# Optimization experiments

Hardware: AMD Instinct MI355X
Metric: run time of the kernel (lower is better)

## Reference

```python
import jax, jax.numpy as jnp
import numpy as np

H, C, PQ, PV, CZ, CS = 12, 16, 4, 8, 128, 384
W_C = (2.0 / (9.0 * PQ)) ** 0.5
INV_SQRT3 = 3.0 ** -0.5


def setup_inputs() -> dict:
    key = jax.random.key(0)
    ks = jax.random.split(key, 20)
    B, N = 2, 512
    s = jax.random.normal(ks[0], (B, N, CS), jnp.float32)
    z = jax.random.normal(ks[1], (B, N, N, CZ), jnp.float32)
    m = jax.random.normal(ks[2], (B, N, 3, 3), jnp.float32)
    rot, _ = jnp.linalg.qr(m)  # proper-ish rotations (orthonormal frames)
    trans = jax.random.normal(ks[3], (B, N, 3), jnp.float32)
    seq_mask = jnp.ones((B, N), jnp.float32)
    sc = 0.02
    params = {
        'Wq': jax.random.normal(ks[4], (CS, H * C)) * sc,
        'bq': jnp.zeros((H * C,)),
        'Wkv': jax.random.normal(ks[5], (CS, H * C * 2)) * sc,
        'bkv': jnp.zeros((H * C * 2,)),
        'Wb': jax.random.normal(ks[6], (CZ, H)) * sc,
        'bb': jnp.zeros((H,)),
        'Wqp': jax.random.normal(ks[7], (CS, 3 * PQ * H)) * sc,
        'bqp': jnp.zeros((3 * PQ * H,)),
        'Wkvp': jax.random.normal(ks[8], (CS, 3 * (PQ + PV) * H)) * sc,
        'bkvp': jnp.zeros((3 * (PQ + PV) * H,)),
        'gamma': jnp.zeros((H,)),
        'Wout': jax.random.normal(ks[9], ((CZ + C + PV * 4) * H, CS)) * sc,
        'bout': jnp.zeros((CS,)),
    }
    return dict(s=s, z=z, rot=rot, trans=trans, seq_mask=seq_mask, **params)


def reference(s, z, rot, trans, seq_mask, Wq, bq, Wkv, bkv, Wb, bb, Wqp, bqp, Wkvp, bkvp, gamma, Wout, bout):
    B, N, _ = s.shape
    # scalar q/k/v
    q = (s @ Wq + bq).reshape(B, N, H, C)
    kv = (s @ Wkv + bkv).reshape(B, N, H, 2 * C)
    k, v = kv[..., :C], kv[..., C:]
    qp = s @ Wqp + bqp                                   # (B,N,3*PQ*H)
    qp = jnp.stack(jnp.split(qp, 3, axis=-1), axis=-1)   # (B,N,PQ*H,3)
    qp = jnp.einsum('bixy,bipy->bipx', rot, qp) + trans[:, :, None, :]
    qp = qp.reshape(B, N, H, PQ, 3)
    # key/value points
    kvp = s @ Wkvp + bkvp
    kvp = jnp.stack(jnp.split(kvp, 3, axis=-1), axis=-1)  # (B,N,(PQ+PV)*H,3)
    kvp = jnp.einsum('bixy,bipy->bipx', rot, kvp) + trans[:, :, None, :]
    kvp = kvp.reshape(B, N, H, PQ + PV, 3)
    kp, vp = kvp[..., :PQ, :], kvp[..., PQ:, :]
    # attention logits: scalar term + pair bias + point-distance term
    bpair = (z @ Wb + bb).transpose(0, 3, 1, 2)          # (B,H,i,j)
    a = jnp.einsum('bihc,bjhc->bhij', q, k) * (3 * C) ** -0.5 + INV_SQRT3 * bpair
    d2 = jnp.sum((qp[:, :, None] - kp[:, None]) ** 2, axis=-1)   # (B,i,j,H,PQ)
    pa = -0.5 * jnp.sum(d2, axis=-1)                      # (B,i,j,H)
    head_w = jax.nn.softplus(gamma)
    pa = pa * (head_w * W_C * INV_SQRT3)
    a = a + pa.transpose(0, 3, 1, 2)
    mask_bias = 100000.0 * (seq_mask[:, :, None] * seq_mask[:, None, :] - 1.0)
    a = a + mask_bias[:, None, :, :]
    a = jax.nn.softmax(a, axis=-1)                        # (B,H,i,j)
    # outputs: scalar values, rotated points (inverse frame), pair features
    o = jnp.einsum('bhij,bjhc->bihc', a, v).reshape(B, N, H * C)
    op = jnp.einsum('bhij,bjhpx->bihpx', a, vp)           # (B,i,H,PV,3)
    op = jnp.einsum('biyx,bihpy->bihpx', rot, op - trans[:, :, None, None, :])  # R^T(p-t)
    onorm = jnp.maximum(jnp.sqrt(jnp.sum(op ** 2, axis=-1)), 1e-6).reshape(B, N, H * PV)
    op = op.reshape(B, N, H * PV, 3)
    opair = jnp.einsum('bhij,bijc->bihc', a, z).reshape(B, N, H * CZ)
    feat = jnp.concatenate([o, op[..., 0], op[..., 1], op[..., 2], onorm, opair], axis=-1)
    return feat @ Wout + bout
```

## Files before the change

### kernel.cpp

```cpp
#include <hip/hip_runtime.h>
#include <hip/hip_bf16.h>

constexpr int B = 2, N = 512, H = 12, C = 16, PQ = 4, PV = 8, CZ = 128, CS = 384;
constexpr int HC   = H * C;
constexpr int FEAT = (CZ + C + PV * 4) * H;
constexpr float QK_SCALE  = 0.14433756729740643f;
constexpr float INV_SQRT3 = 0.5773502691896258f;
constexpr float WC_IS3    = 0.13608276348795434f;

using f32x4 = __attribute__((ext_vector_type(4))) float;
using s16x8 = __attribute__((ext_vector_type(8))) short;

__device__ __forceinline__ short f2b(float f) {
    union { __hip_bfloat16 b; short s; } u;
    u.b = __float2bfloat16(f);
    return u.s;
}
__device__ __forceinline__ float b2f(short s) {
    union { short s; __hip_bfloat16 b; } u;
    u.s = s;
    return __bfloat162float(u.b);
}

constexpr int RPB = 2;

__global__ __launch_bounds__(256) void k_proj(
    const float* __restrict__ s, const float* __restrict__ rot, const float* __restrict__ trans,
    const float* __restrict__ Wq, const float* __restrict__ bq,
    const float* __restrict__ Wkv, const float* __restrict__ bkv,
    const float* __restrict__ Wqp, const float* __restrict__ bqp,
    const float* __restrict__ Wkvp, const float* __restrict__ bkvp,
    const float* __restrict__ gamma, const float* __restrict__ bb,
    const float* __restrict__ Wout,
    short* __restrict__ qcw, short* __restrict__ kkp,
    float* __restrict__ vw, float* __restrict__ vpw,
    short* __restrict__ pcw, float* __restrict__ auxw,
    short* __restrict__ WT)
{
    __shared__ float s_s[RPB][CS];
    __shared__ float rawqp_s[RPB][144];
    __shared__ float rawkvp_s[RPB][432];
    __shared__ float qrot_s[RPB][48][3];
    __shared__ float sq_s[RPB][48];
    __shared__ float R_s[RPB][9], T_s[RPB][3];
    const int t = threadIdx.x;
    const int bi0 = blockIdx.x * RPB;

    for (int idx = t; idx < RPB * CS / 4; idx += 256) {
        int r = idx / (CS / 4), k4 = idx % (CS / 4);
        ((float4*)s_s[r])[k4] = ((const float4*)(s + (size_t)(bi0 + r) * CS))[k4];
    }
    if (t < RPB * 9) R_s[t / 9][t % 9] = rot[bi0 * 9 + t];
    if (t < RPB * 3) T_s[t / 3][t % 3] = trans[bi0 * 3 + t];
    __syncthreads();

    for (int qd = t; qd < 288; qd += 256) {
        const int c = qd * 4;
        const float* Wp; int ldw; const float* bp;
        int seg;
        if (c < 192)      { Wp = Wq   + c;        ldw = 192; bp = bq + c;        seg = 0; }
        else if (c < 576) { Wp = Wkv  + (c - 192); ldw = 384; bp = bkv + (c - 192); seg = 1; }
        else if (c < 720) { Wp = Wqp  + (c - 576); ldw = 144; bp = bqp + (c - 576); seg = 2; }
        else              { Wp = Wkvp + (c - 720); ldw = 432; bp = bkvp + (c - 720); seg = 3; }
        float4 bv = *(const float4*)bp;
        float acc[RPB][4];
        #pragma unroll
        for (int r = 0; r < RPB; ++r) {
            acc[r][0] = bv.x; acc[r][1] = bv.y; acc[r][2] = bv.z; acc[r][3] = bv.w;
        }
        for (int k4 = 0; k4 < CS / 4; ++k4) {
            float4 sv[RPB];
            #pragma unroll
            for (int r = 0; r < RPB; ++r) sv[r] = *(const float4*)&s_s[r][k4 * 4];
            #pragma unroll
            for (int e = 0; e < 4; ++e) {
                float4 wv = *(const float4*)(Wp + (size_t)(k4 * 4 + e) * ldw);
                #pragma unroll
                for (int r = 0; r < RPB; ++r) {
                    float se = ((const float*)&sv[r])[e];
                    acc[r][0] += se * wv.x; acc[r][1] += se * wv.y;
                    acc[r][2] += se * wv.z; acc[r][3] += se * wv.w;
                }
            }
        }
        if (seg == 0) {
            #pragma unroll
            for (int r = 0; r < RPB; ++r) {
                short4 o = make_short4(f2b(QK_SCALE * acc[r][0]), f2b(QK_SCALE * acc[r][1]),
                                       f2b(QK_SCALE * acc[r][2]), f2b(QK_SCALE * acc[r][3]));
                *(short4*)&qcw[(size_t)(bi0 + r) * 192 + c] = o;
            }
        } else if (seg == 1) {
            int cc = c - 192, h = cc >> 5, w5 = cc & 31;
            if (w5 < 16) {
                #pragma unroll
                for (int r = 0; r < RPB; ++r) {
                    short4 o = make_short4(f2b(acc[r][0]), f2b(acc[r][1]),
                                           f2b(acc[r][2]), f2b(acc[r][3]));
                    *(short4*)&kkp[(size_t)(bi0 + r) * 384 + h * 16 + w5] = o;
                }
            } else {
                #pragma unroll
                for (int r = 0; r < RPB; ++r) {
                    int row = bi0 + r;
                    *(float4*)&vw[(size_t)row * 192 + h * 16 + (w5 - 16)] =
                        (float4){acc[r][0], acc[r][1], acc[r][2], acc[r][3]};
                }
            }
        } else if (seg == 2) {
            #pragma unroll
            for (int r = 0; r < RPB; ++r)
                *(float4*)&rawqp_s[r][c - 576] = (float4){acc[r][0], acc[r][1], acc[r][2], acc[r][3]};
        } else {
            #pragma unroll
            for (int r = 0; r < RPB; ++r)
                *(float4*)&rawkvp_s[r][c - 720] = (float4){acc[r][0], acc[r][1], acc[r][2], acc[r][3]};
        }
    }
    __syncthreads();

    for (int idx = t; idx < RPB * 48; idx += 256) {
        int r = idx / 48, p = idx % 48;
        float y0 = rawqp_s[r][p], y1 = rawqp_s[r][48 + p], y2 = rawqp_s[r][96 + p];
        #pragma unroll
        for (int x = 0; x < 3; ++x)
            qrot_s[r][p][x] = T_s[r][x] + R_s[r][x * 3] * y0 + R_s[r][x * 3 + 1] * y1 + R_s[r][x * 3 + 2] * y2;
    }
    for (int idx = t; idx < RPB * 144; idx += 256) {
        int r = idx / 144, p = idx % 144, h = p / 12, pp = p % 12;
        float y0 = rawkvp_s[r][p], y1 = rawkvp_s[r][144 + p], y2 = rawkvp_s[r][288 + p];
        float vals[3]; float ss = 0.0f;
        #pragma unroll
        for (int x = 0; x < 3; ++x) {
            float v = T_s[r][x] + R_s[r][x * 3] * y0 + R_s[r][x * 3 + 1] * y1 + R_s[r][x * 3 + 2] * y2;
            vals[x] = v; ss += v * v;
        }
        int row = bi0 + r;
        if (pp < PQ) {
            #pragma unroll
            for (int x = 0; x < 3; ++x)
                kkp[(size_t)row * 384 + 192 + h * 16 + pp * 3 + x] = f2b(vals[x]);
            sq_s[r][h * 4 + pp] = ss;
        } else {
            #pragma unroll
            for (int x = 0; x < 3; ++x)
                vpw[(size_t)row * 288 + h * 24 + (pp - PQ) * 3 + x] = vals[x];
        }
    }
    __syncthreads();

    if (t < RPB * 12) {
        int r = t / 12, h = t % 12, row = bi0 + r;
        float g = gamma[h];
        float sp = fmaxf(g, 0.0f) + log1pf(expf(-fabsf(g)));
        float pac = -0.5f * sp * WC_IS3;
        float kpsq = sq_s[r][h * 4] + sq_s[r][h * 4 + 1] + sq_s[r][h * 4 + 2] + sq_s[r][h * 4 + 3];
        kkp[(size_t)row * 384 + 192 + h * 16 + 12] = f2b(kpsq);
        kkp[(size_t)row * 384 + 192 + h * 16 + 13] = 0;
        kkp[(size_t)row * 384 + 192 + h * 16 + 14] = 0;
        kkp[(size_t)row * 384 + 192 + h * 16 + 15] = 0;
        float qpsq = 0.0f;
        #pragma unroll
        for (int pq = 0; pq < 4; ++pq)
            #pragma unroll
            for (int x = 0; x < 3; ++x) {
                float qv = qrot_s[r][h * 4 + pq][x];
                qpsq += qv * qv;
                pcw[(size_t)row * 192 + h * 16 + pq * 3 + x] = f2b(-2.0f * pac * qv);
            }
        pcw[(size_t)row * 192 + h * 16 + 12] = f2b(pac);
        pcw[(size_t)row * 192 + h * 16 + 13] = 0;
        pcw[(size_t)row * 192 + h * 16 + 14] = 0;
        pcw[(size_t)row * 192 + h * 16 + 15] = 0;
        auxw[(size_t)row * 16 + h] = INV_SQRT3 * bb[h] + pac * qpsq;
    }
    if (t >= RPB * 12 && t < RPB * 16) {
        int r = (t - RPB * 12) >> 2, hh = 12 + ((t - RPB * 12) & 3);
        auxw[(size_t)(bi0 + r) * 16 + hh] = 0.0f;
    }

    short* tileb = (short*)&s_s[0][0];
    for (int tile = blockIdx.x; tile < 66 * 12; tile += 512) {
        const int k0 = (tile % 66) * 32;
        const int c0 = (tile / 66) * 32;
        __syncthreads();
        {
            int r = t >> 3, c4 = (t & 7) * 4;
            float4 v = *(const float4*)&Wout[(size_t)(k0 + r) * CS + c0 + c4];
            tileb[(c4 + 0) * 33 + r] = f2b(v.x);
            tileb[(c4 + 1) * 33 + r] = f2b(v.y);
            tileb[(c4 + 2) * 33 + r] = f2b(v.z);
            tileb[(c4 + 3) * 33 + r] = f2b(v.w);
        }
        __syncthreads();
        {
            int rr = t >> 3, k4 = (t & 7) * 4;
            short4 o = make_short4(tileb[rr * 33 + k4], tileb[rr * 33 + k4 + 1],
                                   tileb[rr * 33 + k4 + 2], tileb[rr * 33 + k4 + 3]);
            *(short4*)&WT[(size_t)(c0 + rr) * FEAT + k0 + k4] = o;
        }
    }
}

constexpr int PLS = 520;
constexpr int BSEL = 56;

#define LOADZ(BUF, PTR)                                                  \
    {                                                                    \
        _Pragma("unroll")                                                \
        for (int k4 = 0; k4 < 4; ++k4) {                                 \
            BUF[k4 * 2]     = *(const float4*)((PTR) + k4 * 32);         \
            BUF[k4 * 2 + 1] = *(const float4*)((PTR) + k4 * 32 + 4);     \
        }                                                                \
    }

#define COMPUTE(BUF, JC, KPTR)                                                     \
    {                                                                              \
        s16x8 zf[4];                                                               \
        _Pragma("unroll")                                                          \
        for (int kk = 0; kk < 4; ++kk) {                                           \
            float4 u0 = BUF[kk * 2], u1 = BUF[kk * 2 + 1];                         \
            s16x8 f;                                                               \
            f[0] = f2b(u0.x); f[1] = f2b(u0.y); f[2] = f2b(u0.z); f[3] = f2b(u0.w);\
            f[4] = f2b(u1.x); f[5] = f2b(u1.y); f[6] = f2b(u1.z); f[7] = f2b(u1.w);\
            zf[kk] = f;                                                            \
        }                                                                          \
        f32x4 accA = (f32x4){0, 0, 0, 0}, accB = (f32x4){0, 0, 0, 0};              \
        f32x4 accC = (f32x4){0, 0, 0, 0}, accD = (f32x4){0, 0, 0, 0};              \
        _Pragma("unroll")                                                          \
        for (int kk = 0; kk < 4; ++kk) {                                           \
            s16x8 wb = *(const s16x8*)(bl + kk * 8);                               \
            accA = __builtin_amdgcn_mfma_f32_16x16x32_bf16(zf[kk], wb, accA, 0, 0, 0);\
        }                                                                          \
        s16x8 qselr = *(const s16x8*)(bl + 32);                                    \
        s16x8 pselr = *(const s16x8*)(bl + 40);                                    \
        _Pragma("unroll")                                                          \
        for (int kk = 0; kk < 4; ++kk) {                                           \
            s16x8 af = *(const s16x8*)((KPTR) + kk * 32);                          \
            s16x8 bsel = (kk == half) ? qselr : z8;                                \
            accB = __builtin_amdgcn_mfma_f32_16x16x32_bf16(af, bsel, accB, 0, 0, 0); \
        }                                                                          \
        _Pragma("unroll")                                                          \
        for (int kk = 4; kk < 8; ++kk) {                                           \
            s16x8 af = *(const s16x8*)((KPTR) + kk * 32);                          \
            s16x8 bsel;                                                            \
            if (kk < 6) bsel = (kk == half) ? qselr : z8;                          \
            else        bsel = ((kk - 6) == half) ? pselr : z8;                    \
            accC = __builtin_amdgcn_mfma_f32_16x16x32_bf16(af, bsel, accC, 0, 0, 0); \
        }                                                                          \
        _Pragma("unroll")                                                          \
        for (int kk = 8; kk < 12; ++kk) {                                          \
            s16x8 af = *(const s16x8*)((KPTR) + kk * 32);                          \
            s16x8 bsel = ((kk - 6) == half) ? pselr : z8;                          \
            accD = __builtin_amdgcn_mfma_f32_16x16x32_bf16(af, bsel, accD, 0, 0, 0); \
        }                                                                          \
        f32x4 acc = (accA + accB) + (accC + accD);                                 \
        float4 m4 = *(const float4*)(mkp + (JC) * 16);                             \
        float lo[4]; float cm = -INFINITY;                                         \
        _Pragma("unroll")                                                          \
        for (int r = 0; r < 4; ++r) {                                              \
            lo[r] = acc[r] + constH + 100000.0f * (mask_i * ((const float*)&m4)[r] - 1.0f); \
            cm = fmaxf(cm, lo[r]);                                                 \
        }                                                                          \
        cm = fmaxf(cm, __shfl_xor(cm, 16, 64));                                    \
        cm = fmaxf(cm, __shfl_xor(cm, 32, 64));                                    \
        float mnew = fmaxf(m_run, cm);                                             \
        float sc = __expf(m_run - mnew);                                           \
        m_run = mnew;                                                              \
        float p[4]; float ps = 0.0f;                                               \
        _Pragma("unroll")                                                          \
        for (int r = 0; r < 4; ++r) { p[r] = __expf(lo[r] - mnew); ps += p[r]; }   \
        ps += __shfl_xor(ps, 16, 64);                                              \
        ps += __shfl_xor(ps, 32, 64);                                              \
        l_run = l_run * sc + ps;                                                   \
        if (sc != 1.0f) {                                                          \
            for (int jj = lg * 4; jj < (JC) * 16; jj += 16) {                      \
                short* pr = &P_lds[m15 * PLS + jw + jj];                           \
                _Pragma("unroll")                                                  \
                for (int r = 0; r < 4; ++r) pr[r] = f2b(b2f(pr[r]) * sc);          \
            }                                                                      \
        }                                                                          \
        *(short4*)&P_lds[m15 * PLS + jw + (JC) * 16 + lg * 4] =                    \
            make_short4(f2b(p[0]), f2b(p[1]), f2b(p[2]), f2b(p[3]));               \
    }

__global__ __launch_bounds__(256) void k_attn2(
    const float* __restrict__ z, const float* __restrict__ rot, const float* __restrict__ trans,
    const float* __restrict__ seq_mask,
    const float* __restrict__ Wb,
    const short* __restrict__ qcw, const short* __restrict__ kkp,
    const short* __restrict__ pcw, const float* __restrict__ auxw,
    const float* __restrict__ vw, const float* __restrict__ vpw,
    short* __restrict__ featb)
{
    __shared__ short P_lds[16 * PLS];
    __shared__ __align__(16) short bsel_lds[64 * BSEL];
    __shared__ float ml_s[4][16], ll_s[4][16], M_s[16], Linv_s[16];
    __shared__ float ored_s[4][192];
    __shared__ float opred_s[3][288];
    __shared__ float op_f[288];
    __shared__ float R_s[9], T_s[3];

    const int t = threadIdx.x;
    const int w   = t >> 6;
    const int l   = t & 63;
    const int lg  = l >> 4;
    const int m15 = l & 15;
    const int bi  = blockIdx.x;
    const int b   = bi >> 9;
    const int i   = bi & (N - 1);

    if (t < 9) R_s[t] = rot[bi * 9 + t];
    if (t < 3) T_s[t] = trans[bi * 3 + t];

    const bool hv = (m15 < 12);
    const int hcl = hv ? m15 : 0;
    const int half = m15 >> 1;
    const float constH = auxw[(size_t)bi * 16 + m15];
    const float mask_i = seq_mask[bi];

    if (w == 0) {
        short* dst = &bsel_lds[l * BSEL];
        #pragma unroll
        for (int kk = 0; kk < 4; ++kk)
            #pragma unroll
            for (int e = 0; e < 8; ++e) {
                int c = kk * 32 + lg * 8 + e;
                dst[kk * 8 + e] = f2b(hv ? INV_SQRT3 * Wb[c * H + hcl] : 0.0f);
            }
        const bool selh = ((lg >> 1) == (m15 & 1));
        const s16x8 z8v = {0, 0, 0, 0, 0, 0, 0, 0};
        const short* qrow = qcw + (size_t)bi * 192 + hcl * 16;
        s16x8 qlo = *(const s16x8*)qrow;
        s16x8 qhi = *(const s16x8*)(qrow + 8);
        s16x8 q = (hv && selh) ? ((lg & 1) ? qhi : qlo) : z8v;
        const short* prow = pcw + (size_t)bi * 192 + hcl * 16;
        s16x8 plo = *(const s16x8*)prow;
        s16x8 phi = *(const s16x8*)(prow + 8);
        s16x8 p = (hv && selh) ? ((lg & 1) ? phi : plo) : z8v;
        *(s16x8*)(dst + 32) = q;
        *(s16x8*)(dst + 40) = p;
    }
    __syncthreads();

    float m_run = -INFINITY, l_run = 0.0f;

    const size_t zbase = ((size_t)b * N + i) * (size_t)(N * CZ);
    const int jw = w * 128;
    const float* zAp = z + zbase + (size_t)(jw + m15) * CZ + lg * 8;
    const short* kAp = kkp + (size_t)(b * N + jw + m15) * 384 + lg * 8;
    const float* mkp = seq_mask + b * N + jw + lg * 4;
    const short* bl = &bsel_lds[l * BSEL];
    const s16x8 z8 = {0, 0, 0, 0, 0, 0, 0, 0};

    float4 bufA[8], bufB[8], bufC[8];
    LOADZ(bufA, zAp);
    LOADZ(bufB, zAp + 16 * CZ);
    LOADZ(bufC, zAp + 32 * CZ);   COMPUTE(bufA, 0, kAp); kAp += 6144;
    LOADZ(bufA, zAp + 48 * CZ);   COMPUTE(bufB, 1, kAp); kAp += 6144;
    LOADZ(bufB, zAp + 64 * CZ);   COMPUTE(bufC, 2, kAp); kAp += 6144;
    LOADZ(bufC, zAp + 80 * CZ);   COMPUTE(bufA, 3, kAp); kAp += 6144;
    LOADZ(bufA, zAp + 96 * CZ);   COMPUTE(bufB, 4, kAp); kAp += 6144;
    LOADZ(bufB, zAp + 112 * CZ);  COMPUTE(bufC, 5, kAp); kAp += 6144;
    COMPUTE(bufA, 6, kAp); kAp += 6144;
    COMPUTE(bufB, 7, kAp);

    if (lg == 0) { ml_s[w][m15] = m_run; ll_s[w][m15] = l_run; }
    __syncthreads();
    if (t < 16) {
        float M = ml_s[0][t];
        M = fmaxf(M, ml_s[1][t]); M = fmaxf(M, ml_s[2][t]); M = fmaxf(M, ml_s[3][t]);
        float Lt = 0.0f;
        #pragma unroll
        for (int ww = 0; ww < 4; ++ww) Lt += ll_s[ww][t] * __expf(ml_s[ww][t] - M);
        M_s[t] = M;
        Linv_s[t] = 1.0f / Lt;
    }
    __syncthreads();

    {
        const int h = t >> 4, j0t = (t & 15) * 32;
        const int wv = j0t >> 7;
        const float sS = __expf(ml_s[wv][h] - M_s[h]) * Linv_s[h];
        #pragma unroll
        for (int k = 0; k < 4; ++k) {
            s16x8 v = *(const s16x8*)&P_lds[h * PLS + j0t + k * 8];
            s16x8 o;
            #pragma unroll
            for (int e = 0; e < 8; ++e) o[e] = f2b(b2f(v[e]) * sS);
            *(s16x8*)&P_lds[h * PLS + j0t + k * 8] = o;
        }
    }
    __syncthreads();

    short* F = featb + (size_t)bi * FEAT;

    f32x4 oa0 = (f32x4){0, 0, 0, 0}, oa1 = (f32x4){0, 0, 0, 0};
    const int c0 = w * 32;
    #pragma unroll 4
    for (int kk = 0; kk < 16; ++kk) {
        s16x8 af = *(const s16x8*)&P_lds[m15 * PLS + kk * 32 + lg * 8];
        const float* zb = z + zbase + (size_t)(kk * 32 + lg * 8) * CZ + c0 + m15;
        s16x8 b0f, b1f;
        #pragma unroll
        for (int e = 0; e < 8; ++e) {
            b0f[e] = f2b(zb[(size_t)e * CZ]);
            b1f[e] = f2b(zb[(size_t)e * CZ + 16]);
        }
        oa0 = __builtin_amdgcn_mfma_f32_16x16x32_bf16(af, b0f, oa0, 0, 0, 0);
        oa1 = __builtin_amdgcn_mfma_f32_16x16x32_bf16(af, b1f, oa1, 0, 0, 0);
    }
    #pragma unroll
    for (int r = 0; r < 4; ++r) {
        int h = lg * 4 + r;
        if (h < 12) {
            F[576 + h * 128 + c0 + m15]      = f2b(oa0[r]);
            F[576 + h * 128 + c0 + 16 + m15] = f2b(oa1[r]);
        }
    }

    if (t < 192) {
        const int c4 = t % 48, jg = t / 48;
        const int h = c4 >> 2;
        const short* Pr = &P_lds[h * PLS + jg * 128];
        const float* vb = vw + ((size_t)b * N + jg * 128) * 192 + c4 * 4;
        f32x4 a = (f32x4){0, 0, 0, 0};
        #pragma unroll 2
        for (int q = 0; q < 16; ++q) {
            s16x8 pv = *(const s16x8*)(Pr + q * 8);
            #pragma unroll
            for (int e = 0; e < 8; ++e) {
                float4 v4 = *(const float4*)(vb + (size_t)(q * 8 + e) * 192);
                float pj = b2f(pv[e]);
                a[0] += pj * v4.x; a[1] += pj * v4.y; a[2] += pj * v4.z; a[3] += pj * v4.w;
            }
        }
        *(f32x4*)&ored_s[jg][c4 * 4] = a;
    }

    if (t < 216) {
        const int c4 = t % 72, jg = t / 72;
        const int h = c4 / 6;
        const int j0g = (jg == 0) ? 0 : (jg == 1 ? 176 : 352);
        const int nq = (jg == 2) ? 20 : 22;
        const short* Pr = &P_lds[h * PLS + j0g];
        const float* vb = vpw + ((size_t)b * N + j0g) * 288 + c4 * 4;
        f32x4 a = (f32x4){0, 0, 0, 0};
        #pragma unroll 2
        for (int q = 0; q < nq; ++q) {
            s16x8 pv = *(const s16x8*)(Pr + q * 8);
            #pragma unroll
            for (int e = 0; e < 8; ++e) {
                float4 v4 = *(const float4*)(vb + (size_t)(q * 8 + e) * 288);
                float pj = b2f(pv[e]);
                a[0] += pj * v4.x; a[1] += pj * v4.y; a[2] += pj * v4.z; a[3] += pj * v4.w;
            }
        }
        *(f32x4*)&opred_s[jg][c4 * 4] = a;
    }
    __syncthreads();

    if (t < 192)
        F[t] = f2b(ored_s[0][t] + ored_s[1][t] + ored_s[2][t] + ored_s[3][t]);
    if (t < 72) {
        #pragma unroll
        for (int x = 0; x < 4; ++x) {
            int rv = t * 4 + x;
            op_f[rv] = opred_s[0][rv] + opred_s[1][rv] + opred_s[2][rv];
        }
    }
    __syncthreads();

    if (t < 96) {
        float o0 = op_f[t * 3 + 0] - T_s[0];
        float o1 = op_f[t * 3 + 1] - T_s[1];
        float o2 = op_f[t * 3 + 2] - T_s[2];
        float n2 = 0.0f;
        #pragma unroll
        for (int x = 0; x < 3; ++x) {
            float rx = R_s[0 * 3 + x] * o0 + R_s[1 * 3 + x] * o1 + R_s[2 * 3 + x] * o2;
            F[HC + 96 * x + t] = f2b(rx);
            n2 += rx * rx;
        }
        F[480 + t] = f2b(fmaxf(sqrtf(n2), 1e-6f));
    }
}

__global__ __launch_bounds__(256) void k_out(
    const short* __restrict__ featb, const short* __restrict__ WT,
    const float* __restrict__ bout, float* __restrict__ out)
{
    __shared__ short A_s[32 * 40];
    __shared__ short B_s[64 * 40];
    const int t = threadIdx.x;
    const int w   = t >> 6;
    const int l   = t & 63;
    const int lg  = l >> 4;
    const int m15 = l & 15;
    const int wm = w >> 1, wn = w & 1;
    const int bm = (blockIdx.x / 6) * 32;
    const int bn = (blockIdx.x % 6) * 64;

    f32x4 acc[2];
    acc[0] = (f32x4){0, 0, 0, 0};
    acc[1] = (f32x4){0, 0, 0, 0};

    const int sr = t >> 2;
    const int sk = (t & 3) * 8;

    s16x8 rA, rB;
    if (t < 128) rA = *(const s16x8*)&featb[(size_t)(bm + sr) * FEAT + sk];
    rB = *(const s16x8*)&WT[(size_t)(bn + sr) * FEAT + sk];

    for (int k0 = 0; k0 < FEAT; k0 += 32) {
        __syncthreads();
        if (t < 128) *(s16x8*)&A_s[sr * 40 + sk] = rA;
        *(s16x8*)&B_s[sr * 40 + sk] = rB;
        __syncthreads();

        const int kn = k0 + 32;
        if (kn < FEAT) {
            if (t < 128) rA = *(const s16x8*)&featb[(size_t)(bm + sr) * FEAT + kn + sk];
            rB = *(const s16x8*)&WT[(size_t)(bn + sr) * FEAT + kn + sk];
        }

        s16x8 af = *(const s16x8*)&A_s[(wm * 16 + m15) * 40 + lg * 8];
        #pragma unroll
        for (int sn = 0; sn < 2; ++sn) {
            s16x8 bf = *(const s16x8*)&B_s[(wn * 32 + sn * 16 + m15) * 40 + lg * 8];
            acc[sn] = __builtin_amdgcn_mfma_f32_16x16x32_bf16(af, bf, acc[sn], 0, 0, 0);
        }
    }

    #pragma unroll
    for (int sn = 0; sn < 2; ++sn) {
        int col = bn + wn * 32 + sn * 16 + m15;
        float bo = bout[col];
        #pragma unroll
        for (int r = 0; r < 4; ++r) {
            int row = bm + wm * 16 + lg * 4 + r;
            out[(size_t)row * CS + col] = acc[sn][r] + bo;
        }
    }
}

extern "C" void kernel_launch(void* const* d_in, const int* in_sizes, int n_in,
                              void* d_out, int out_size, void* d_ws, size_t ws_size,
                              hipStream_t stream)
{
    const float* s     = (const float*)d_in[0];
    const float* z     = (const float*)d_in[1];
    const float* rot   = (const float*)d_in[2];
    const float* trans = (const float*)d_in[3];
    const float* mask  = (const float*)d_in[4];
    const float* Wq    = (const float*)d_in[5];
    const float* bq    = (const float*)d_in[6];
    const float* Wkv   = (const float*)d_in[7];
    const float* bkv   = (const float*)d_in[8];
    const float* Wb    = (const float*)d_in[9];
    const float* bb    = (const float*)d_in[10];
    const float* Wqp   = (const float*)d_in[11];
    const float* bqp   = (const float*)d_in[12];
    const float* Wkvp  = (const float*)d_in[13];
    const float* bkvp  = (const float*)d_in[14];
    const float* gamma = (const float*)d_in[15];
    const float* Wout  = (const float*)d_in[16];
    const float* bout  = (const float*)d_in[17];

    char* wsb = (char*)d_ws;
    short* featb = (short*)wsb;
    float* vw    = (float*)(wsb + 4325376);
    float* vpw   = (float*)(wsb + 5111808);
    float* auxw  = (float*)(wsb + 6291456);
    short* qcw   = (short*)(wsb + 6356992);
    short* pcw   = (short*)(wsb + 6750208);
    short* kkp   = (short*)(wsb + 7143424);
    short* WT    = (short*)(wsb + 7929856);

    hipLaunchKernelGGL(k_proj, dim3(B * N / RPB), dim3(256), 0, stream,
                       s, rot, trans, Wq, bq, Wkv, bkv, Wqp, bqp, Wkvp, bkvp,
                       gamma, bb, Wout, qcw, kkp, vw, vpw, pcw, auxw, WT);
    hipLaunchKernelGGL(k_attn2, dim3(B * N), dim3(256), 0, stream,
                       z, rot, trans, mask, Wb, qcw, kkp, pcw, auxw, vw, vpw, featb);
    hipLaunchKernelGGL(k_out, dim3(96 * 2), dim3(256), 0, stream,
                       featb, WT, bout, (float*)d_out);
}
```

Baseline: 279.1 us.

## Cut z prefetch to double buffering and alias LDS scratch to raise occupancy

The z-tile prefetch in the attention kernel drops from three register buffers to two and moves into a loop. The bsel, ored, opred and op_f shared arrays now share one overlaid LDS region, since their lifetimes do not overlap. Both changes lower register and LDS use per block so more blocks can be resident at once. In exchange, each load has less time in flight to hide latency. The overlay also relies on bsel being dead before the reductions write into the same bytes. The last loop iteration reloads an already-consumed tile into bufA, which is redundant but harmless.

```diff
diff --git a/kernel.cpp b/kernel.cpp
--- a/kernel.cpp
+++ b/kernel.cpp
@@ -294,11 +294,12 @@
     short* __restrict__ featb)
 {
     __shared__ short P_lds[16 * PLS];
-    __shared__ __align__(16) short bsel_lds[64 * BSEL];
+    __shared__ __align__(16) char ovl[7680];
+    short* bsel_lds = (short*)ovl;
+    float* ored_s   = (float*)ovl;
+    float* opred_s  = (float*)(ovl + 3072);
+    float* op_f     = (float*)(ovl + 6528);
     __shared__ float ml_s[4][16], ll_s[4][16], M_s[16], Linv_s[16];
-    __shared__ float ored_s[4][192];
-    __shared__ float opred_s[3][288];
-    __shared__ float op_f[288];
     __shared__ float R_s[9], T_s[3];
 
     const int t = threadIdx.x;
@@ -353,17 +354,21 @@
     const short* bl = &bsel_lds[l * BSEL];
     const s16x8 z8 = {0, 0, 0, 0, 0, 0, 0, 0};
 
-    float4 bufA[8], bufB[8], bufC[8];
+    float4 bufA[8], bufB[8];
     LOADZ(bufA, zAp);
-    LOADZ(bufB, zAp + 16 * CZ);
-    LOADZ(bufC, zAp + 32 * CZ);   COMPUTE(bufA, 0, kAp); kAp += 6144;
-    LOADZ(bufA, zAp + 48 * CZ);   COMPUTE(bufB, 1, kAp); kAp += 6144;
-    LOADZ(bufB, zAp + 64 * CZ);   COMPUTE(bufC, 2, kAp); kAp += 6144;
-    LOADZ(bufC, zAp + 80 * CZ);   COMPUTE(bufA, 3, kAp); kAp += 6144;
-    LOADZ(bufA, zAp + 96 * CZ);   COMPUTE(bufB, 4, kAp); kAp += 6144;
-    LOADZ(bufB, zAp + 112 * CZ);  COMPUTE(bufC, 5, kAp); kAp += 6144;
-    COMPUTE(bufA, 6, kAp); kAp += 6144;
-    COMPUTE(bufB, 7, kAp);
+
+    for (int jc2 = 0; jc2 < 8; jc2 += 2) {
+        LOADZ(bufB, zAp + 16 * CZ);
+        COMPUTE(bufA, jc2, kAp);
+        kAp += 6144;
+        {
+            const float* nx = zAp + ((jc2 == 6) ? (16 * CZ) : (32 * CZ));
+            LOADZ(bufA, nx);
+        }
+        COMPUTE(bufB, jc2 + 1, kAp);
+        kAp += 6144;
+        zAp += 32 * CZ;
+    }
 
     if (lg == 0) { ml_s[w][m15] = m_run; ll_s[w][m15] = l_run; }
     __syncthreads();
@@ -435,7 +440,7 @@
                 a[0] += pj * v4.x; a[1] += pj * v4.y; a[2] += pj * v4.z; a[3] += pj * v4.w;
             }
         }
-        *(f32x4*)&ored_s[jg][c4 * 4] = a;
+        *(f32x4*)&ored_s[jg * 192 + c4 * 4] = a;
     }
 
     if (t < 216) {
@@ -456,17 +461,17 @@
                 a[0] += pj * v4.x; a[1] += pj * v4.y; a[2] += pj * v4.z; a[3] += pj * v4.w;
             }
         }
-        *(f32x4*)&opred_s[jg][c4 * 4] = a;
+        *(f32x4*)&opred_s[jg * 288 + c4 * 4] = a;
     }
     __syncthreads();
 
     if (t < 192)
-        F[t] = f2b(ored_s[0][t] + ored_s[1][t] + ored_s[2][t] + ored_s[3][t]);
+        F[t] = f2b(ored_s[t] + ored_s[192 + t] + ored_s[384 + t] + ored_s[576 + t]);
     if (t < 72) {
         #pragma unroll
         for (int x = 0; x < 4; ++x) {
             int rv = t * 4 + x;
-            op_f[rv] = opred_s[0][rv] + opred_s[1][rv] + opred_s[2][rv];
+            op_f[rv] = opred_s[rv] + opred_s[288 + rv] + opred_s[576 + rv];
         }
     }
     __syncthreads();
```

Result: no change. 279.2 us (+0.0%).
